# Kernel tuning notes

Hardware: AMD Instinct MI355X
Metric: run time of the kernel (lower is better)

## Reference

```python
import jax, jax.numpy as jnp
import numpy as np

DIM_MODEL = 1024
DIM_K = 1024
DIM_V = 1024


def setup_inputs() -> dict:
    key = jax.random.key(0)
    ks = jax.random.split(key, 7)
    B, S = 4, 2048
    scale = 1.0 / np.sqrt(DIM_MODEL)
    return {
        "x": jax.random.normal(ks[0], (B, S, DIM_MODEL), dtype=jnp.float32),
        # weights stored [in, out] (transpose of torch Linear.weight)
        "Wq": jax.random.normal(ks[1], (DIM_MODEL, DIM_K), dtype=jnp.float32) * scale,
        "Wk": jax.random.normal(ks[2], (DIM_MODEL, DIM_K), dtype=jnp.float32) * scale,
        "Wv": jax.random.normal(ks[3], (DIM_MODEL, DIM_V), dtype=jnp.float32) * scale,
        "Wo": jax.random.normal(ks[4], (DIM_V, DIM_MODEL), dtype=jnp.float32) * (1.0 / np.sqrt(DIM_V)),
        "ln2_gamma": jnp.ones((DIM_MODEL,), dtype=jnp.float32),
        "ln2_beta": jnp.zeros((DIM_MODEL,), dtype=jnp.float32),
    }


def _layernorm(x, gamma, beta, eps=1e-5):
    mu = jnp.mean(x, axis=-1, keepdims=True)
    var = jnp.var(x, axis=-1, keepdims=True)
    return (x - mu) * jax.lax.rsqrt(var + eps) * gamma + beta


def reference(x, Wq, Wk, Wv, Wo, ln2_gamma, ln2_beta):
    # single-head attention, x: [B,S,D]
    q = jnp.einsum("bsd,dk->bsk", x, Wq)
    k = jnp.einsum("bsd,dk->bsk", x, Wk)
    v = jnp.einsum("bsd,dv->bsv", x, Wv)
    scores = jnp.einsum("bqk,bsk->bqs", q, k) / jnp.sqrt(jnp.asarray(DIM_K, x.dtype))
    attn = jax.nn.softmax(scores, axis=-1)  # [B,S,S]
    ctx = jnp.einsum("bqs,bsv->bqv", attn, v)
    hidden = jnp.einsum("bqv,vd->bqd", ctx, Wo)
    hidden = _layernorm(hidden, ln2_gamma, ln2_beta)
    return hidden
```

## Files before the change

### kernel.cpp

```cpp
#include <hip/hip_runtime.h>
#include <hip/hip_bf16.h>
#include <stdint.h>

typedef __bf16 bf16;
typedef __attribute__((ext_vector_type(8))) __bf16 bf16x8;
typedef __attribute__((ext_vector_type(4))) __bf16 bf16x4;
typedef __attribute__((ext_vector_type(4))) float f32x4;

#define AS1 __attribute__((address_space(1)))
#define AS3 __attribute__((address_space(3)))

#define LDX 1088
#define LDS2 2112

__device__ __forceinline__ void gl_lds16(const void* g, void* l) {
  __builtin_amdgcn_global_load_lds((const AS1 uint32_t*)g, (AS3 uint32_t*)l, 16, 0, 0);
}

template <int MODE>
__global__ __launch_bounds__(256) void gemm128(
    const bf16* __restrict__ Abase, const bf16* __restrict__ Bbase,
    bf16* __restrict__ Cbase, int K, int lda, int ldb, int ldc,
    long long sA, long long sB, long long sC, float alpha,
    float* __restrict__ lsum, bf16* __restrict__ C2, bf16* __restrict__ C3) {
  extern __shared__ char smem[];
  const int z = blockIdx.z;
  const bf16* A = Abase + (long long)z * sA;
  const bf16* B = Bbase + (long long)z * sB;
  bf16* C = Cbase + (long long)z * sC;
  const int m0 = blockIdx.y * 128, n0 = blockIdx.x * 128;
  const int t = threadIdx.x;
  const int lane = t & 63, wave = t >> 6;
  const int wm = (wave >> 1) * 64, wn = (wave & 1) * 64;
  const int quad = lane >> 4, r = lane & 15;

  const int srow = t >> 3;
  const int schunk = (t & 7) ^ (srow & 7);
  const bf16* ga = A + (long long)(m0 + srow) * lda + schunk * 8;
  const bf16* gb = B + (long long)(n0 + srow) * ldb + schunk * 8;
  char* la = smem + t * 16;
  char* lb = smem + 16384 + t * 16;

  f32x4 acc[4][4] = {};

  for (int k0 = 0; k0 < K; k0 += 64) {
    __syncthreads();
#pragma unroll
    for (int rd = 0; rd < 4; rd++) {
      gl_lds16(ga + (long long)(32 * rd) * lda, la + rd * 4096);
      gl_lds16(gb + (long long)(32 * rd) * ldb, lb + rd * 4096);
    }
    ga += 64;
    gb += 64;
    __syncthreads();

#pragma unroll
    for (int kk = 0; kk < 2; kk++) {
      bf16x8 af[4], bfr[4];
      const int csa = ((kk * 4 + quad) ^ (r & 7)) * 16;
      const char* pa = smem + (wm + r) * 128 + csa;
      const char* pb = smem + 16384 + (wn + r) * 128 + csa;
#pragma unroll
      for (int i = 0; i < 4; i++) af[i] = *(const bf16x8*)(pa + i * 2048);
#pragma unroll
      for (int j = 0; j < 4; j++) bfr[j] = *(const bf16x8*)(pb + j * 2048);
#pragma unroll
      for (int i = 0; i < 4; i++)
#pragma unroll
        for (int j = 0; j < 4; j++)
          acc[i][j] = __builtin_amdgcn_mfma_f32_16x16x32_bf16(af[i], bfr[j],
                                                              acc[i][j], 0, 0, 0);
    }
  }

  if constexpr (MODE == 4) {
    bf16* dst;
    int c0;
    if (n0 < 1024) {
      dst = Cbase; c0 = n0;
    } else if (n0 < 2048) {
      dst = C2; c0 = n0 - 1024;
    } else {
      dst = C3; c0 = n0 - 2048;
    }
#pragma unroll
    for (int i = 0; i < 4; i++) {
      const int row0 = m0 + wm + i * 16 + quad * 4;
#pragma unroll
      for (int j = 0; j < 4; j++) {
        const int col = c0 + wn + j * 16 + r;
#pragma unroll
        for (int rg = 0; rg < 4; rg++)
          dst[(long long)(row0 + rg) * ldc + col] = (bf16)acc[i][j][rg];
      }
    }
    return;
  }

#pragma unroll
  for (int i = 0; i < 4; i++) {
    const int row0 = m0 + wm + i * 16 + quad * 4;
    float rsum[4] = {0.f, 0.f, 0.f, 0.f};
    float inv[4];
    if constexpr (MODE == 2) {
#pragma unroll
      for (int rg = 0; rg < 4; rg++)
        inv[rg] = 1.f / lsum[(long long)z * 2048 + row0 + rg];
    }
#pragma unroll
    for (int j = 0; j < 4; j++) {
      const int col = n0 + wn + j * 16 + r;
#pragma unroll
      for (int rg = 0; rg < 4; rg++) {
        float v = acc[i][j][rg] * alpha;
        if constexpr (MODE == 1) {
          bf16 eb = (bf16)__expf(v);
          C[(long long)(row0 + rg) * ldc + col] = eb;
          rsum[rg] += (float)eb;
        } else if constexpr (MODE == 2) {
          C[(long long)(row0 + rg) * ldc + col] = (bf16)(v * inv[rg]);
        } else {
          C[(long long)(row0 + rg) * ldc + col] = (bf16)v;
        }
      }
    }
    if constexpr (MODE == 1) {
#pragma unroll
      for (int rg = 0; rg < 4; rg++) {
#pragma unroll
        for (int off = 8; off >= 1; off >>= 1)
          rsum[rg] += __shfl_xor(rsum[rg], off);
        if (r == 0)
          atomicAdd(&lsum[(long long)z * 2048 + row0 + rg], rsum[rg]);
      }
    }
  }
}

__global__ __launch_bounds__(256) void prep(
    const float* __restrict__ x, const float* __restrict__ Wq,
    const float* __restrict__ Wk, const float* __restrict__ Wv,
    const float* __restrict__ Wo, bf16* __restrict__ Xb,
    bf16* __restrict__ Wcat, bf16* __restrict__ Wot,
    float* __restrict__ lsum) {
  __shared__ float tile[32][33];
  const int bx = blockIdx.x;
  const int t = threadIdx.x;
  if (bx < 4096) {
    if (bx < 32) lsum[bx * 256 + t] = 0.f;
    const int row = bx * 2 + (t >> 7);
    const int col = (t & 127) * 8;
    const float4* p = (const float4*)(x + (long long)row * 1024 + col);
    float4 a = p[0], b = p[1];
    bf16x8 o;
    o[0] = (bf16)a.x; o[1] = (bf16)a.y; o[2] = (bf16)a.z; o[3] = (bf16)a.w;
    o[4] = (bf16)b.x; o[5] = (bf16)b.y; o[6] = (bf16)b.z; o[7] = (bf16)b.w;
    *(bf16x8*)(Xb + (long long)row * LDX + col) = o;
  } else {
    int idx = bx - 4096;
    const int zw = idx >> 10;
    idx &= 1023;
    const int tiy = idx >> 5, tix = idx & 31;
    const float* W = (zw == 0) ? Wq : (zw == 1) ? Wk : (zw == 2) ? Wv : Wo;
    bf16* dst = (zw < 3) ? (Wcat + (long long)zw * 1024 * LDX) : Wot;
    const int bx0 = tix * 32, by0 = tiy * 32;
    const int ttx = t & 31, tty = t >> 5;
#pragma unroll
    for (int i = 0; i < 32; i += 8)
      tile[tty + i][ttx] = W[(long long)(by0 + tty + i) * 1024 + bx0 + ttx];
    __syncthreads();
#pragma unroll
    for (int i = 0; i < 32; i += 8)
      dst[(long long)(bx0 + tty + i) * LDX + by0 + ttx] = (bf16)tile[ttx][tty + i];
  }
}

__global__ __launch_bounds__(256) void layernorm_rows(
    const bf16* __restrict__ H, const float* __restrict__ gamma,
    const float* __restrict__ beta, float* __restrict__ O) {
  const long long row = blockIdx.x;
  const bf16* h = H + row * 1024;
  float* o = O + row * 1024;
  const int t = threadIdx.x;
  const int lane = t & 63, wave = t >> 6;
  bf16x4 hv = ((const bf16x4*)h)[t];
  float v[4] = {(float)hv[0], (float)hv[1], (float)hv[2], (float)hv[3]};
  float s = v[0] + v[1] + v[2] + v[3];
  float ss = v[0] * v[0] + v[1] * v[1] + v[2] * v[2] + v[3] * v[3];
#pragma unroll
  for (int off = 32; off >= 1; off >>= 1) {
    s += __shfl_xor(s, off);
    ss += __shfl_xor(ss, off);
  }
  __shared__ float rs[4], rss[4];
  if (lane == 0) {
    rs[wave] = s;
    rss[wave] = ss;
  }
  __syncthreads();
  s = rs[0] + rs[1] + rs[2] + rs[3];
  ss = rss[0] + rss[1] + rss[2] + rss[3];
  const float mean = s * (1.f / 1024.f);
  const float var = ss * (1.f / 1024.f) - mean * mean;
  const float rstd = rsqrtf(var + 1e-5f);
  float4 g = ((const float4*)gamma)[t];
  float4 bb = ((const float4*)beta)[t];
  float4 rr;
  rr.x = (v[0] - mean) * rstd * g.x + bb.x;
  rr.y = (v[1] - mean) * rstd * g.y + bb.y;
  rr.z = (v[2] - mean) * rstd * g.z + bb.z;
  rr.w = (v[3] - mean) * rstd * g.w + bb.w;
  ((float4*)o)[t] = rr;
}

extern "C" void kernel_launch(void* const* d_in, const int* in_sizes, int n_in,
                              void* d_out, int out_size, void* d_ws,
                              size_t ws_size, hipStream_t stream) {
  const float* x = (const float*)d_in[0];
  const float* Wq = (const float*)d_in[1];
  const float* Wk = (const float*)d_in[2];
  const float* Wv = (const float*)d_in[3];
  const float* Wo = (const float*)d_in[4];
  const float* gamma = (const float*)d_in[5];
  const float* beta = (const float*)d_in[6];
  float* out = (float*)d_out;

  char* ws = (char*)d_ws;
  const size_t MB = 1024ull * 1024ull;
  bf16* Xb = (bf16*)(ws + 0);
  bf16* Wcat = (bf16*)(ws + 18 * MB);
  bf16* Wot = (bf16*)(ws + 25 * MB);
  bf16* Qd = (bf16*)(ws + 28 * MB);
  bf16* Kd = (bf16*)(ws + 46 * MB);
  bf16* Vd = (bf16*)(ws + 64 * MB);
  bf16* expS = (bf16*)(ws + 82 * MB);
  float* lsum = (float*)(ws + 117 * MB);
  bf16* VWo = (bf16*)(ws + 118 * MB);
  bf16* Hd = (bf16*)(ws + 136 * MB);

  prep<<<8192, 256, 0, stream>>>(x, Wq, Wk, Wv, Wo, Xb, Wcat, Wot, lsum);

  gemm128<4><<<dim3(24, 64, 1), 256, 32768, stream>>>(
      Xb, Wcat, Qd, 1024, LDX, LDX, LDX, 0, 0, 0, 1.f, nullptr, Kd, Vd);

  gemm128<1><<<dim3(16, 16, 4), 256, 32768, stream>>>(
      Qd, Kd, expS, 1024, LDX, LDX, LDS2, 2048LL * LDX, 2048LL * LDX,
      2048LL * LDS2, 0.03125f, lsum, nullptr, nullptr);

  gemm128<0><<<dim3(16, 8, 4), 256, 32768, stream>>>(
      Wot, Vd, VWo, 1024, LDX, LDX, LDS2, 0, 2048LL * LDX, 1024LL * LDS2,
      1.f, nullptr, nullptr, nullptr);

  gemm128<2><<<dim3(8, 16, 4), 256, 32768, stream>>>(
      expS, VWo, Hd, 2048, LDS2, LDS2, 1024, 2048LL * LDS2, 1024LL * LDS2,
      2048LL * 1024, 1.f, lsum, nullptr, nullptr);

  layernorm_rows<<<8192, 256, 0, stream>>>(Hd, gamma, beta, out);
}
```

Baseline: 290.2 us.

## Merge scores and V·Wo GEMMs, shrink hidden tile, fuse LN stats into epilogue

The scores GEMM and the V·Wo GEMM, which are independent, now run in one launch selected by block index. This removes a kernel boundary and lets the two fill the GPU together. The final GEMM uses a 64-row tile so it launches twice as many blocks, and its epilogue accumulates per-row sum and sum-of-squares with atomics. The layernorm kernel then skips its reduction. The cost is extra atomics and less reuse per block in the final GEMM. The layernorm statistics are now computed from fp32 values rather than the rounded bf16 values.

Measured after the change: 287.7 us. Within noise of the previous version (-0.8%).

```diff
diff --git a/kernel.cpp b/kernel.cpp
--- a/kernel.cpp
+++ b/kernel.cpp
@@ -17,55 +17,52 @@
   __builtin_amdgcn_global_load_lds((const AS1 uint32_t*)g, (AS3 uint32_t*)l, 16, 0, 0);
 }
 
-template <int MODE>
-__global__ __launch_bounds__(256) void gemm128(
-    const bf16* __restrict__ Abase, const bf16* __restrict__ Bbase,
-    bf16* __restrict__ Cbase, int K, int lda, int ldb, int ldc,
-    long long sA, long long sB, long long sC, float alpha,
-    float* __restrict__ lsum, bf16* __restrict__ C2, bf16* __restrict__ C3) {
-  extern __shared__ char smem[];
-  const int z = blockIdx.z;
-  const bf16* A = Abase + (long long)z * sA;
-  const bf16* B = Bbase + (long long)z * sB;
-  bf16* C = Cbase + (long long)z * sC;
-  const int m0 = blockIdx.y * 128, n0 = blockIdx.x * 128;
+template <int MODE, int WMT>
+__device__ __forceinline__ void gemm_body(
+    const bf16* __restrict__ A, const bf16* __restrict__ B,
+    bf16* __restrict__ C, bf16* __restrict__ C2, bf16* __restrict__ C3,
+    int K, int lda, int ldb, int ldc, float alpha,
+    float* __restrict__ lsum_z, float* __restrict__ stats_z,
+    char* smem, int m0, int n0) {
   const int t = threadIdx.x;
   const int lane = t & 63, wave = t >> 6;
-  const int wm = (wave >> 1) * 64, wn = (wave & 1) * 64;
+  const int wm = (wave >> 1) * (WMT * 16), wn = (wave & 1) * 64;
   const int quad = lane >> 4, r = lane & 15;
+  const int BM = WMT * 32;
 
   const int srow = t >> 3;
   const int schunk = (t & 7) ^ (srow & 7);
   const bf16* ga = A + (long long)(m0 + srow) * lda + schunk * 8;
   const bf16* gb = B + (long long)(n0 + srow) * ldb + schunk * 8;
   char* la = smem + t * 16;
-  char* lb = smem + 16384 + t * 16;
-
-  f32x4 acc[4][4] = {};
+  char* lb = smem + BM * 128 + t * 16;
+
+  f32x4 acc[WMT][4] = {};
 
   for (int k0 = 0; k0 < K; k0 += 64) {
     __syncthreads();
 #pragma unroll
-    for (int rd = 0; rd < 4; rd++) {
+    for (int rd = 0; rd < WMT; rd++)
       gl_lds16(ga + (long long)(32 * rd) * lda, la + rd * 4096);
+#pragma unroll
+    for (int rd = 0; rd < 4; rd++)
       gl_lds16(gb + (long long)(32 * rd) * ldb, lb + rd * 4096);
-    }
     ga += 64;
     gb += 64;
     __syncthreads();
 
 #pragma unroll
     for (int kk = 0; kk < 2; kk++) {
-      bf16x8 af[4], bfr[4];
+      bf16x8 af[WMT], bfr[4];
       const int csa = ((kk * 4 + quad) ^ (r & 7)) * 16;
       const char* pa = smem + (wm + r) * 128 + csa;
-      const char* pb = smem + 16384 + (wn + r) * 128 + csa;
-#pragma unroll
-      for (int i = 0; i < 4; i++) af[i] = *(const bf16x8*)(pa + i * 2048);
+      const char* pb = smem + BM * 128 + (wn + r) * 128 + csa;
+#pragma unroll
+      for (int i = 0; i < WMT; i++) af[i] = *(const bf16x8*)(pa + i * 2048);
 #pragma unroll
       for (int j = 0; j < 4; j++) bfr[j] = *(const bf16x8*)(pb + j * 2048);
 #pragma unroll
-      for (int i = 0; i < 4; i++)
+      for (int i = 0; i < WMT; i++)
 #pragma unroll
         for (int j = 0; j < 4; j++)
           acc[i][j] = __builtin_amdgcn_mfma_f32_16x16x32_bf16(af[i], bfr[j],
@@ -77,14 +74,14 @@
     bf16* dst;
     int c0;
     if (n0 < 1024) {
-      dst = Cbase; c0 = n0;
+      dst = C; c0 = n0;
     } else if (n0 < 2048) {
       dst = C2; c0 = n0 - 1024;
     } else {
       dst = C3; c0 = n0 - 2048;
     }
 #pragma unroll
-    for (int i = 0; i < 4; i++) {
+    for (int i = 0; i < WMT; i++) {
       const int row0 = m0 + wm + i * 16 + quad * 4;
 #pragma unroll
       for (int j = 0; j < 4; j++) {
@@ -98,14 +95,14 @@
   }
 
 #pragma unroll
-  for (int i = 0; i < 4; i++) {
+  for (int i = 0; i < WMT; i++) {
     const int row0 = m0 + wm + i * 16 + quad * 4;
     float rsum[4] = {0.f, 0.f, 0.f, 0.f};
+    float s2sum[4] = {0.f, 0.f, 0.f, 0.f};
     float inv[4];
     if constexpr (MODE == 2) {
 #pragma unroll
-      for (int rg = 0; rg < 4; rg++)
-        inv[rg] = 1.f / lsum[(long long)z * 2048 + row0 + rg];
+      for (int rg = 0; rg < 4; rg++) inv[rg] = 1.f / lsum_z[row0 + rg];
     }
 #pragma unroll
     for (int j = 0; j < 4; j++) {
@@ -118,7 +115,10 @@
           C[(long long)(row0 + rg) * ldc + col] = eb;
           rsum[rg] += (float)eb;
         } else if constexpr (MODE == 2) {
-          C[(long long)(row0 + rg) * ldc + col] = (bf16)(v * inv[rg]);
+          v *= inv[rg];
+          C[(long long)(row0 + rg) * ldc + col] = (bf16)v;
+          rsum[rg] += v;
+          s2sum[rg] += v * v;
         } else {
           C[(long long)(row0 + rg) * ldc + col] = (bf16)v;
         }
@@ -130,11 +130,69 @@
 #pragma unroll
         for (int off = 8; off >= 1; off >>= 1)
           rsum[rg] += __shfl_xor(rsum[rg], off);
-        if (r == 0)
-          atomicAdd(&lsum[(long long)z * 2048 + row0 + rg], rsum[rg]);
-      }
-    }
-  }
+        if (r == 0) atomicAdd(&lsum_z[row0 + rg], rsum[rg]);
+      }
+    }
+    if constexpr (MODE == 2) {
+#pragma unroll
+      for (int rg = 0; rg < 4; rg++) {
+#pragma unroll
+        for (int off = 8; off >= 1; off >>= 1) {
+          rsum[rg] += __shfl_xor(rsum[rg], off);
+          s2sum[rg] += __shfl_xor(s2sum[rg], off);
+        }
+        if (r == 0) {
+          atomicAdd(&stats_z[2 * (row0 + rg)], rsum[rg]);
+          atomicAdd(&stats_z[2 * (row0 + rg) + 1], s2sum[rg]);
+        }
+      }
+    }
+  }
+}
+
+__global__ __launch_bounds__(256) void qkv_gemm(
+    const bf16* __restrict__ Xb, const bf16* __restrict__ Wcat,
+    bf16* __restrict__ Qd, bf16* __restrict__ Kd, bf16* __restrict__ Vd) {
+  extern __shared__ char smem[];
+  gemm_body<4, 4>(Xb, Wcat, Qd, Kd, Vd, 1024, LDX, LDX, LDX, 1.f, nullptr,
+                  nullptr, smem, blockIdx.y * 128, blockIdx.x * 128);
+}
+
+__global__ __launch_bounds__(256) void scores_vwo(
+    const bf16* __restrict__ Qd, const bf16* __restrict__ Kd,
+    bf16* __restrict__ expS, float* __restrict__ lsum,
+    const bf16* __restrict__ Wot, const bf16* __restrict__ Vd,
+    bf16* __restrict__ VWo) {
+  extern __shared__ char smem[];
+  const int bid = blockIdx.x;
+  if (bid < 1024) {
+    const int z = bid >> 8, rem = bid & 255;
+    gemm_body<1, 4>(Qd + (long long)z * 2048 * LDX,
+                    Kd + (long long)z * 2048 * LDX,
+                    expS + (long long)z * 2048 * LDS2, nullptr, nullptr, 1024,
+                    LDX, LDX, LDS2, 0.03125f, lsum + z * 2048, nullptr, smem,
+                    (rem >> 4) * 128, (rem & 15) * 128);
+  } else {
+    const int idx = bid - 1024;
+    const int z = idx >> 7, rem = idx & 127;
+    gemm_body<0, 4>(Wot, Vd + (long long)z * 2048 * LDX,
+                    VWo + (long long)z * 1024 * LDS2, nullptr, nullptr, 1024,
+                    LDX, LDX, LDS2, 1.f, nullptr, nullptr, smem,
+                    (rem >> 4) * 128, (rem & 15) * 128);
+  }
+}
+
+__global__ __launch_bounds__(256) void hidden_gemm(
+    const bf16* __restrict__ expS, const bf16* __restrict__ VWo,
+    bf16* __restrict__ Hd, float* __restrict__ lsum,
+    float* __restrict__ stats) {
+  extern __shared__ char smem[];
+  const int z = blockIdx.z;
+  gemm_body<2, 2>(expS + (long long)z * 2048 * LDS2,
+                  VWo + (long long)z * 1024 * LDS2,
+                  Hd + (long long)z * 2048 * 1024, nullptr, nullptr, 2048,
+                  LDS2, LDS2, 1024, 1.f, lsum + z * 2048, stats + z * 4096,
+                  smem, blockIdx.y * 64, blockIdx.x * 128);
 }
 
 __global__ __launch_bounds__(256) void prep(
@@ -142,12 +200,13 @@
     const float* __restrict__ Wk, const float* __restrict__ Wv,
     const float* __restrict__ Wo, bf16* __restrict__ Xb,
     bf16* __restrict__ Wcat, bf16* __restrict__ Wot,
-    float* __restrict__ lsum) {
+    float* __restrict__ lsum, float* __restrict__ stats) {
   __shared__ float tile[32][33];
   const int bx = blockIdx.x;
   const int t = threadIdx.x;
   if (bx < 4096) {
     if (bx < 32) lsum[bx * 256 + t] = 0.f;
+    else if (bx < 96) stats[(bx - 32) * 256 + t] = 0.f;
     const int row = bx * 2 + (t >> 7);
     const int col = (t & 127) * 8;
     const float4* p = (const float4*)(x + (long long)row * 1024 + col);
@@ -176,40 +235,24 @@
 }
 
 __global__ __launch_bounds__(256) void layernorm_rows(
-    const bf16* __restrict__ H, const float* __restrict__ gamma,
-    const float* __restrict__ beta, float* __restrict__ O) {
+    const bf16* __restrict__ H, const float* __restrict__ stats,
+    const float* __restrict__ gamma, const float* __restrict__ beta,
+    float* __restrict__ O) {
   const long long row = blockIdx.x;
   const bf16* h = H + row * 1024;
   float* o = O + row * 1024;
   const int t = threadIdx.x;
-  const int lane = t & 63, wave = t >> 6;
+  const float mean = stats[2 * row] * (1.f / 1024.f);
+  const float var = stats[2 * row + 1] * (1.f / 1024.f) - mean * mean;
+  const float rstd = rsqrtf(var + 1e-5f);
   bf16x4 hv = ((const bf16x4*)h)[t];
-  float v[4] = {(float)hv[0], (float)hv[1], (float)hv[2], (float)hv[3]};
-  float s = v[0] + v[1] + v[2] + v[3];
-  float ss = v[0] * v[0] + v[1] * v[1] + v[2] * v[2] + v[3] * v[3];
-#pragma unroll
-  for (int off = 32; off >= 1; off >>= 1) {
-    s += __shfl_xor(s, off);
-    ss += __shfl_xor(ss, off);
-  }
-  __shared__ float rs[4], rss[4];
-  if (lane == 0) {
-    rs[wave] = s;
-    rss[wave] = ss;
-  }
-  __syncthreads();
-  s = rs[0] + rs[1] + rs[2] + rs[3];
-  ss = rss[0] + rss[1] + rss[2] + rss[3];
-  const float mean = s * (1.f / 1024.f);
-  const float var = ss * (1.f / 1024.f) - mean * mean;
-  const float rstd = rsqrtf(var + 1e-5f);
   float4 g = ((const float4*)gamma)[t];
   float4 bb = ((const float4*)beta)[t];
   float4 rr;
-  rr.x = (v[0] - mean) * rstd * g.x + bb.x;
-  rr.y = (v[1] - mean) * rstd * g.y + bb.y;
-  rr.z = (v[2] - mean) * rstd * g.z + bb.z;
-  rr.w = (v[3] - mean) * rstd * g.w + bb.w;
+  rr.x = ((float)hv[0] - mean) * rstd * g.x + bb.x;
+  rr.y = ((float)hv[1] - mean) * rstd * g.y + bb.y;
+  rr.z = ((float)hv[2] - mean) * rstd * g.z + bb.z;
+  rr.w = ((float)hv[3] - mean) * rstd * g.w + bb.w;
   ((float4*)o)[t] = rr;
 }
 
@@ -235,25 +278,19 @@
   bf16* Vd = (bf16*)(ws + 64 * MB);
   bf16* expS = (bf16*)(ws + 82 * MB);
   float* lsum = (float*)(ws + 117 * MB);
+  float* stats = (float*)(ws + 117 * MB + 64 * 1024);
   bf16* VWo = (bf16*)(ws + 118 * MB);
   bf16* Hd = (bf16*)(ws + 136 * MB);
 
-  prep<<<8192, 256, 0, stream>>>(x, Wq, Wk, Wv, Wo, Xb, Wcat, Wot, lsum);
-
-  gemm128<4><<<dim3(24, 64, 1), 256, 32768, stream>>>(
-      Xb, Wcat, Qd, 1024, LDX, LDX, LDX, 0, 0, 0, 1.f, nullptr, Kd, Vd);
-
-  gemm128<1><<<dim3(16, 16, 4), 256, 32768, stream>>>(
-      Qd, Kd, expS, 1024, LDX, LDX, LDS2, 2048LL * LDX, 2048LL * LDX,
-      2048LL * LDS2, 0.03125f, lsum, nullptr, nullptr);
-
-  gemm128<0><<<dim3(16, 8, 4), 256, 32768, stream>>>(
-      Wot, Vd, VWo, 1024, LDX, LDX, LDS2, 0, 2048LL * LDX, 1024LL * LDS2,
-      1.f, nullptr, nullptr, nullptr);
-
-  gemm128<2><<<dim3(8, 16, 4), 256, 32768, stream>>>(
-      expS, VWo, Hd, 2048, LDS2, LDS2, 1024, 2048LL * LDS2, 1024LL * LDS2,
-      2048LL * 1024, 1.f, lsum, nullptr, nullptr);
-
-  layernorm_rows<<<8192, 256, 0, stream>>>(Hd, gamma, beta, out);
-}
+  prep<<<8192, 256, 0, stream>>>(x, Wq, Wk, Wv, Wo, Xb, Wcat, Wot, lsum,
+                                 stats);
+
+  qkv_gemm<<<dim3(24, 64), 256, 32768, stream>>>(Xb, Wcat, Qd, Kd, Vd);
+
+  scores_vwo<<<1536, 256, 32768, stream>>>(Qd, Kd, expS, lsum, Wot, Vd, VWo);
+
+  hidden_gemm<<<dim3(8, 32, 4), 256, 24576, stream>>>(expS, VWo, Hd, lsum,
+                                                      stats);
+
+  layernorm_rows<<<8192, 256, 0, stream>>>(Hd, stats, gamma, beta, out);
+}
```
